# Kernel optimization log

Hardware: AMD Instinct MI355X
Metric: run time of the kernel (lower is better)

## Reference

```python
import jax, jax.numpy as jnp
import numpy as np

N, E, D, H, L = 50000, 800000, 64, 1, 4
R_DIMS = [64, 32, 16, 16]
LN_EPS = 1e-6  # flax LayerNorm default


def _ln(x, s, b):
    m = jnp.mean(x, axis=-1, keepdims=True)
    v = jnp.mean(jnp.square(x - m), axis=-1, keepdims=True)
    return (x - m) / jnp.sqrt(v + LN_EPS) * s + b


def _jat_layer(x, edges, senders, receivers, mask, Wq, Wk, Wa, ln_s, ln_b, readout):
    # x: (N, H, D) node features
    n = x.shape[0]
    q = jnp.einsum('nab,abcd->ncd', x, Wq)   # (N, H, D) query projection
    k = jnp.einsum('nab,abcd->ncd', x, Wk)   # (N, H, D) key projection
    sq = q[senders]                           # (E, H, D) gather by sender
    rk = k[receivers]                         # (E, H, D) gather by receiver
    feat = jax.nn.swish(sq + rk)
    # per-head edge distance powers, as in the original code
    ep = jnp.reshape(jnp.stack([jnp.power(edges, i + 1) for i in range(H)], axis=0), (-1, H, 1))
    feat = jnp.concatenate([feat, ep], axis=-1)       # (E, H, D+1)
    logits = jnp.einsum('eab,abcd->ecd', feat, Wa)    # (E, H, 1)
    logits = logits + jnp.reshape(jnp.where(mask, 0.0, -jnp.inf), (-1, 1, 1))
    # segment softmax over receiver segments (stable)
    maxs = jax.ops.segment_max(logits, receivers, n)
    w = jnp.exp(logits - maxs[receivers])
    w = w / jax.ops.segment_sum(w, receivers, n)[receivers]
    new = jax.ops.segment_sum(sq * w, receivers, n)   # (N, H, D)
    new = jax.nn.swish(new) + x  # skip_proj is identity (same n_head, dim)
    if not readout:
        new = _ln(new, ln_s, ln_b)
    return new


def setup_inputs() -> dict:
    key = jax.random.key(0)
    ks = jax.random.split(key, 32)
    inp = {
        'nodes': jax.random.normal(ks[0], (N, D), jnp.float32),
        'edges': jax.random.uniform(ks[1], (E, 1), jnp.float32, 0.1, 5.0),
        'senders': jax.random.randint(ks[2], (E,), 0, N, jnp.int32),
        'receivers': jax.random.randint(ks[3], (E,), 0, N, jnp.int32),
        'mask': jnp.ones((E,), bool),
        'Wq': jax.random.normal(ks[4], (L, H, D, H, D), jnp.float32) / np.sqrt(D).astype(np.float32),
        'Wk': jax.random.normal(ks[5], (L, H, D, H, D), jnp.float32) / np.sqrt(D).astype(np.float32),
        'Wa': jax.random.normal(ks[6], (L, H, D + 1, H, 1), jnp.float32) / np.sqrt(D + 1).astype(np.float32),
        'ln_scale': jnp.ones((L - 1, D), jnp.float32),
        'ln_bias': jnp.zeros((L - 1, D), jnp.float32),
    }
    dims = [H * D] + R_DIMS
    for i in range(4):
        inp[f'Wr{i}'] = jax.random.normal(ks[7 + i], (dims[i], dims[i + 1]), jnp.float32) / np.sqrt(dims[i]).astype(np.float32)
        inp[f'rs{i}'] = jnp.ones((dims[i + 1],), jnp.float32)
        inp[f'rb{i}'] = jnp.zeros((dims[i + 1],), jnp.float32)
    inp['Wr4'] = jax.random.normal(ks[11], (R_DIMS[-1], 1), jnp.float32) / np.sqrt(R_DIMS[-1]).astype(np.float32)
    return inp


def reference(nodes, edges, senders, receivers, mask, Wq, Wk, Wa, ln_scale, ln_bias,
              Wr0, Wr1, Wr2, Wr3, Wr4, rs0, rs1, rs2, rs3, rb0, rb1, rb2, rb3):
    x = nodes[:, None, :]  # (N, 1, D): stack to head axis (first layer)
    for l in range(L):
        readout = (l == L - 1)
        ln_s = ln_scale[l] if not readout else None
        ln_b = ln_bias[l] if not readout else None
        x = _jat_layer(x, edges, senders, receivers, mask, Wq[l], Wk[l], Wa[l], ln_s, ln_b, readout)
    # pyramidal readout head [64:32:16:16:1]
    h = jnp.reshape(x, (x.shape[0], -1))
    for Wd, s, b in zip((Wr0, Wr1, Wr2, Wr3), (rs0, rs1, rs2, rs3), (rb0, rb1, rb2, rb3)):
        h = jax.nn.swish(_ln(h @ Wd, s, b))
    return jax.nn.swish(h @ Wr4)  # (N, 1) atomic contributions
```

## Files before the change

### kernel.cpp

```cpp
#include <hip/hip_runtime.h>

#define NN 50000
#define EE 800000

typedef unsigned short ushort_t;
typedef unsigned int uint_t;

__device__ __forceinline__ float swishf(float v) {
    return v / (1.f + __expf(-v));
}
__device__ __forceinline__ ushort_t f2bf(float f) {
    uint_t u = __float_as_uint(f);
    return (ushort_t)((u + 0x7fffu + ((u >> 16) & 1u)) >> 16);
}
__device__ __forceinline__ float bf2f(ushort_t h) {
    return __uint_as_float(((uint_t)h) << 16);
}
__device__ __forceinline__ float rlane(float v, int i) {
    return __int_as_float(__builtin_amdgcn_readlane(__float_as_int(v), i));
}

__global__ void __launch_bounds__(256) qk_kernel(
    const float* __restrict__ x, const float* __restrict__ Wq, const float* __restrict__ Wk,
    ushort_t* __restrict__ qbf, float* __restrict__ k)
{
    const int lane = threadIdx.x & 63;
    const int wave = (blockIdx.x * 256 + threadIdx.x) >> 6;
    const int nw = gridDim.x * 4;
    float wq[64], wk[64];
#pragma unroll
    for (int i = 0; i < 64; ++i) { wq[i] = Wq[i * 64 + lane]; wk[i] = Wk[i * 64 + lane]; }
    for (int row = wave; row < NN; row += nw) {
        const float h = x[(size_t)row * 64 + lane];
        float aq0 = 0.f, aq1 = 0.f, ak0 = 0.f, ak1 = 0.f;
#pragma unroll
        for (int i = 0; i < 64; i += 2) {
            const float h0 = rlane(h, i), h1 = rlane(h, i + 1);
            aq0 = fmaf(h0, wq[i], aq0);     ak0 = fmaf(h0, wk[i], ak0);
            aq1 = fmaf(h1, wq[i + 1], aq1); ak1 = fmaf(h1, wk[i + 1], ak1);
        }
        qbf[(size_t)row * 64 + lane] = f2bf(aq0 + aq1);
        k[(size_t)row * 64 + lane] = ak0 + ak1;
    }
}

__global__ void __launch_bounds__(256) hist_kernel(
    const int* __restrict__ receivers, int* __restrict__ counts)
{
    int e = blockIdx.x * 256 + threadIdx.x;
    int stride = gridDim.x * 256;
    for (; e < EE; e += stride) atomicAdd(counts + receivers[e], 1);
}

__global__ void __launch_bounds__(256) scanA_kernel(
    const int* __restrict__ counts, int* __restrict__ bsum)
{
    const int idx = blockIdx.x * 256 + threadIdx.x;
    const int lane = threadIdx.x & 63;
    const int wid = threadIdx.x >> 6;
    int s = (idx < NN) ? counts[idx] : 0;
#pragma unroll
    for (int m = 32; m; m >>= 1) s += __shfl_xor(s, m);
    __shared__ int ws[4];
    if (lane == 0) ws[wid] = s;
    __syncthreads();
    if (threadIdx.x == 0) bsum[blockIdx.x] = ws[0] + ws[1] + ws[2] + ws[3];
}

__global__ void __launch_bounds__(256) scanB_kernel(
    const int* __restrict__ bsum, int* __restrict__ boff,
    int* __restrict__ offsets, int nb)
{
    __shared__ int ts[256];
    const int t = threadIdx.x;
    const int v = (t < nb) ? bsum[t] : 0;
    ts[t] = v;
    __syncthreads();
#pragma unroll
    for (int d = 1; d < 256; d <<= 1) {
        const int o = (t >= d) ? ts[t - d] : 0;
        __syncthreads();
        ts[t] += o;
        __syncthreads();
    }
    if (t < nb) boff[t] = ts[t] - v;
    if (t == 0) offsets[NN] = EE;
}

__global__ void __launch_bounds__(256) scanC_kernel(
    const int* __restrict__ counts, const int* __restrict__ boff,
    int* __restrict__ offsets)
{
    const int idx = blockIdx.x * 256 + threadIdx.x;
    const int lane = threadIdx.x & 63;
    const int wid = threadIdx.x >> 6;
    const int v = (idx < NN) ? counts[idx] : 0;
    int incl = v;
#pragma unroll
    for (int d = 1; d < 64; d <<= 1) {
        const int o = __shfl_up(incl, d);
        if (lane >= d) incl += o;
    }
    __shared__ int ws[4];
    if (lane == 63) ws[wid] = incl;
    __syncthreads();
    int wpre = 0;
#pragma unroll
    for (int w = 0; w < 4; ++w) wpre += (w < wid) ? ws[w] : 0;
    if (idx < NN) offsets[idx] = boff[blockIdx.x] + wpre + incl - v;
}

__global__ void __launch_bounds__(256) scatter_kernel(
    const int* __restrict__ receivers, const int* __restrict__ senders,
    const float* __restrict__ edges, const int* __restrict__ offsets,
    int* __restrict__ ctr, int* __restrict__ ssort, float* __restrict__ esort)
{
    int e = blockIdx.x * 256 + threadIdx.x;
    int stride = gridDim.x * 256;
    for (; e < EE; e += stride) {
        int r = receivers[e];
        int pos = atomicAdd(ctr + r, 1);
        int idx = offsets[r] + pos;
        ssort[idx] = senders[e];
        esort[idx] = edges[e];
    }
}

__global__ void __launch_bounds__(256) attn_kernel(
    const ushort_t* __restrict__ qbf, const float* __restrict__ k,
    const int* __restrict__ ssort, const float* __restrict__ esort,
    const int* __restrict__ offsets, const float* __restrict__ Wa,
    float* __restrict__ x, const float* __restrict__ ln_s,
    const float* __restrict__ ln_b, int do_ln)
{
    __shared__ ushort_t sQ[4][8][64];
    __shared__ float sWb[4][8];
    const int lane = threadIdx.x & 63;
    const int winb = threadIdx.x >> 6;
    const int wave = (blockIdx.x * 256 + threadIdx.x) >> 6;
    const int nw = gridDim.x * 4;
    const int c = lane & 7;
    const int e = lane >> 3;
    const int ofs = c * 8;
    float wac[8];
#pragma unroll
    for (int j = 0; j < 8; ++j) wac[j] = Wa[ofs + j];
    const float wa64 = Wa[64];
    const float lnsv = ln_s[lane], lnbv = ln_b[lane];

    for (int r = wave; r < NN; r += nw) {
        float kc[8];
        {
            const float4 k0 = *(const float4*)(k + (size_t)r * 64 + ofs);
            const float4 k1 = *(const float4*)(k + (size_t)r * 64 + ofs + 4);
            kc[0] = k0.x; kc[1] = k0.y; kc[2] = k0.z; kc[3] = k0.w;
            kc[4] = k1.x; kc[5] = k1.y; kc[6] = k1.z; kc[7] = k1.w;
        }
        const float xv = x[(size_t)r * 64 + lane];
        const int beg = offsets[r], end = offsets[r + 1];
        float m = -3.0e38f, denp = 0.f, acc = 0.f;

        bool valid = (beg + e) < end;
        int s = 0; float ea = 0.f;
        if (valid) { s = ssort[beg + e]; ea = esort[beg + e]; }
        uint4 qraw = *(const uint4*)(qbf + (size_t)s * 64 + ofs);

        int i0 = beg;
        while (i0 < end) {
            const int ni0 = i0 + 8;
            bool nvalid = false; int ns = 0; float nea = 0.f;
            uint4 nqraw = qraw;
            if (ni0 < end) {
                nvalid = (ni0 + e) < end;
                if (nvalid) { ns = ssort[ni0 + e]; nea = esort[ni0 + e]; }
                nqraw = *(const uint4*)(qbf + (size_t)ns * 64 + ofs);
            }
            float qv[8];
            qv[0] = __uint_as_float(qraw.x << 16);
            qv[1] = __uint_as_float(qraw.x & 0xFFFF0000u);
            qv[2] = __uint_as_float(qraw.y << 16);
            qv[3] = __uint_as_float(qraw.y & 0xFFFF0000u);
            qv[4] = __uint_as_float(qraw.z << 16);
            qv[5] = __uint_as_float(qraw.z & 0xFFFF0000u);
            qv[6] = __uint_as_float(qraw.w << 16);
            qv[7] = __uint_as_float(qraw.w & 0xFFFF0000u);
            float p = 0.f;
#pragma unroll
            for (int j = 0; j < 8; ++j) p = fmaf(swishf(qv[j] + kc[j]), wac[j], p);
            p += __shfl_xor(p, 1);
            p += __shfl_xor(p, 2);
            p += __shfl_xor(p, 4);
            const float logit = valid ? fmaf(ea, wa64, p) : -3.0e38f;
            float cm = logit;
            cm = fmaxf(cm, __shfl_xor(cm, 8));
            cm = fmaxf(cm, __shfl_xor(cm, 16));
            cm = fmaxf(cm, __shfl_xor(cm, 32));
            if (cm > m) {
                const float sc = __expf(m - cm);
                denp *= sc; acc *= sc; m = cm;
            }
            const float w = valid ? __expf(logit - m) : 0.f;
            denp += w;
            *(uint4*)(&sQ[winb][e][ofs]) = qraw;
            if (c == 0) sWb[winb][e] = w;
            __builtin_amdgcn_wave_barrier();
#pragma unroll
            for (int j = 0; j < 8; ++j)
                acc = fmaf(sWb[winb][j], bf2f(sQ[winb][j][lane]), acc);
            __builtin_amdgcn_wave_barrier();
            qraw = nqraw; ea = nea; valid = nvalid; i0 = ni0;
        }

        float den = denp;
#pragma unroll
        for (int msk = 32; msk; msk >>= 1) den += __shfl_xor(den, msk);
        den *= 0.125f;
        float v = den > 0.f ? acc / den : 0.f;
        float nv = swishf(v) + xv;
        if (do_ln) {
            float sum = nv;
#pragma unroll
            for (int msk = 32; msk; msk >>= 1) sum += __shfl_xor(sum, msk);
            const float mean = sum * (1.f / 64.f);
            const float d = nv - mean;
            float vs = d * d;
#pragma unroll
            for (int msk = 32; msk; msk >>= 1) vs += __shfl_xor(vs, msk);
            nv = d * rsqrtf(vs * (1.f / 64.f) + 1e-6f) * lnsv + lnbv;
        }
        x[(size_t)r * 64 + lane] = nv;
    }
}

__device__ __forceinline__ float ln_swish_w(float v, float s, float b) {
    float sum = v, sq = v * v;
#pragma unroll
    for (int m = 32; m; m >>= 1) { sum += __shfl_xor(sum, m); sq += __shfl_xor(sq, m); }
    const float mean = sum * (1.f / 64.f);
    const float var = fmaf(-mean, mean, sq * (1.f / 64.f));
    return swishf((v - mean) * rsqrtf(var + 1e-6f) * s + b);
}

__global__ void __launch_bounds__(256) readout_kernel(
    const float* __restrict__ x,
    const float* __restrict__ W0, const float* __restrict__ rs0, const float* __restrict__ rb0,
    const float* __restrict__ W1, const float* __restrict__ rs1, const float* __restrict__ rb1,
    const float* __restrict__ W2, const float* __restrict__ rs2, const float* __restrict__ rb2,
    const float* __restrict__ W3, const float* __restrict__ rs3, const float* __restrict__ rb3,
    const float* __restrict__ W4, float* __restrict__ out)
{
    const int lane = threadIdx.x & 63;
    const int wave = (blockIdx.x * 256 + threadIdx.x) >> 6;
    const int nw = gridDim.x * 4;
    const int j1 = lane & 31, j2 = lane & 15;
    float w0[64], w1[64], w2[32], w3[16];
#pragma unroll
    for (int i = 0; i < 64; ++i) w0[i] = W0[i * 64 + lane];
#pragma unroll
    for (int i = 0; i < 64; ++i) w1[i] = W1[i * 32 + j1];
#pragma unroll
    for (int i = 0; i < 32; ++i) w2[i] = W2[i * 16 + j2];
#pragma unroll
    for (int i = 0; i < 16; ++i) w3[i] = W3[i * 16 + j2];
    const float w4v = W4[j2];
    const float s0v = rs0[lane], b0v = rb0[lane];
    const float s1v = rs1[j1],  b1v = rb1[j1];
    const float s2v = rs2[j2],  b2v = rb2[j2];
    const float s3v = rs3[j2],  b3v = rb3[j2];

    for (int n = wave; n < NN; n += nw) {
        const float h = x[(size_t)n * 64 + lane];
        float a0 = 0.f, a1 = 0.f, a2 = 0.f, a3 = 0.f;
#pragma unroll
        for (int i = 0; i < 64; i += 4) {
            a0 = fmaf(rlane(h, i),     w0[i],     a0);
            a1 = fmaf(rlane(h, i + 1), w0[i + 1], a1);
            a2 = fmaf(rlane(h, i + 2), w0[i + 2], a2);
            a3 = fmaf(rlane(h, i + 3), w0[i + 3], a3);
        }
        const float y0 = ln_swish_w((a0 + a1) + (a2 + a3), s0v, b0v);

        a0 = a1 = a2 = a3 = 0.f;
#pragma unroll
        for (int i = 0; i < 64; i += 4) {
            a0 = fmaf(rlane(y0, i),     w1[i],     a0);
            a1 = fmaf(rlane(y0, i + 1), w1[i + 1], a1);
            a2 = fmaf(rlane(y0, i + 2), w1[i + 2], a2);
            a3 = fmaf(rlane(y0, i + 3), w1[i + 3], a3);
        }
        const float y1 = ln_swish_w((a0 + a1) + (a2 + a3), s1v, b1v);

        a0 = a1 = a2 = a3 = 0.f;
#pragma unroll
        for (int i = 0; i < 32; i += 4) {
            a0 = fmaf(rlane(y1, i),     w2[i],     a0);
            a1 = fmaf(rlane(y1, i + 1), w2[i + 1], a1);
            a2 = fmaf(rlane(y1, i + 2), w2[i + 2], a2);
            a3 = fmaf(rlane(y1, i + 3), w2[i + 3], a3);
        }
        const float y2 = ln_swish_w((a0 + a1) + (a2 + a3), s2v, b2v);

        a0 = a1 = a2 = a3 = 0.f;
#pragma unroll
        for (int i = 0; i < 16; i += 4) {
            a0 = fmaf(rlane(y2, i),     w3[i],     a0);
            a1 = fmaf(rlane(y2, i + 1), w3[i + 1], a1);
            a2 = fmaf(rlane(y2, i + 2), w3[i + 2], a2);
            a3 = fmaf(rlane(y2, i + 3), w3[i + 3], a3);
        }
        const float y3 = ln_swish_w((a0 + a1) + (a2 + a3), s3v, b3v);

        float p = y3 * w4v;
#pragma unroll
        for (int m = 32; m; m >>= 1) p += __shfl_xor(p, m);
        if (lane == 0) out[n] = swishf(p * 0.25f);
    }
}

extern "C" void kernel_launch(void* const* d_in, const int* in_sizes, int n_in,
                              void* d_out, int out_size, void* d_ws, size_t ws_size,
                              hipStream_t stream)
{
    const float* nodes     = (const float*)d_in[0];
    const float* edges     = (const float*)d_in[1];
    const int*   senders   = (const int*)d_in[2];
    const int*   receivers = (const int*)d_in[3];
    const float* Wq  = (const float*)d_in[5];
    const float* Wk  = (const float*)d_in[6];
    const float* Wa  = (const float*)d_in[7];
    const float* ln_s = (const float*)d_in[8];
    const float* ln_b = (const float*)d_in[9];
    const float* Wr0 = (const float*)d_in[10];
    const float* rs0 = (const float*)d_in[11];
    const float* rb0 = (const float*)d_in[12];
    const float* Wr1 = (const float*)d_in[13];
    const float* rs1 = (const float*)d_in[14];
    const float* rb1 = (const float*)d_in[15];
    const float* Wr2 = (const float*)d_in[16];
    const float* rs2 = (const float*)d_in[17];
    const float* rb2 = (const float*)d_in[18];
    const float* Wr3 = (const float*)d_in[19];
    const float* rs3 = (const float*)d_in[20];
    const float* rb3 = (const float*)d_in[21];
    const float* Wr4 = (const float*)d_in[22];
    float* out = (float*)d_out;

    float*    x       = (float*)d_ws;
    float*    k       = x + (size_t)NN * 64;
    ushort_t* qbf     = (ushort_t*)(k + (size_t)NN * 64);
    int*      counts  = (int*)(qbf + (size_t)NN * 64);
    int*      ctr     = counts + NN;
    int*      offsets = ctr + NN;
    int*      ssort   = offsets + NN + 1;
    float*    esort   = (float*)(ssort + EE);
    int*      bsum    = (int*)(esort + EE);
    int*      boff    = bsum + 256;

    const int NB = (NN + 255) / 256;

    hipMemcpyAsync(x, nodes, (size_t)NN * 64 * sizeof(float), hipMemcpyDeviceToDevice, stream);

    hipMemsetAsync(counts, 0, 2 * NN * sizeof(int), stream);
    hist_kernel<<<3125, 256, 0, stream>>>(receivers, counts);
    scanA_kernel<<<NB, 256, 0, stream>>>(counts, bsum);
    scanB_kernel<<<1, 256, 0, stream>>>(bsum, boff, offsets, NB);
    scanC_kernel<<<NB, 256, 0, stream>>>(counts, boff, offsets);
    scatter_kernel<<<3125, 256, 0, stream>>>(receivers, senders, edges, offsets, ctr, ssort, esort);

    for (int l = 0; l < 4; ++l) {
        qk_kernel<<<1024, 256, 0, stream>>>(x, Wq + l * 4096, Wk + l * 4096, qbf, k);
        int lnidx = l < 3 ? l : 0;
        attn_kernel<<<3125, 256, 0, stream>>>(qbf, k, ssort, esort, offsets,
                                              Wa + l * 65, x,
                                              ln_s + lnidx * 64, ln_b + lnidx * 64,
                                              l < 3 ? 1 : 0);
    }
    readout_kernel<<<1024, 256, 0, stream>>>(x, Wr0, rs0, rb0, Wr1, rs1, rb1,
                                             Wr2, rs2, rb2, Wr3, rs3, rb3, Wr4, out);
}
```

Before: 593.4 us.

## Pack sender/edge into int2, use fast reciprocal, split readout kernel

Packs the sorted sender index and edge value into one int2 array, so the attention loop does one 8-byte load per edge instead of two separate loads. Divisions in swish and in the softmax normalisation are replaced with a hardware reciprocal instruction, and qk gets a launch-bounds occupancy hint. The readout kernel is split into two kernels that pass the first layer's activations through global memory (reusing the k buffer), which lowers register pressure per kernel. The costs are an extra global round trip and launch for the readout, and slightly less precise reciprocals.

```diff
diff --git a/kernel.cpp b/kernel.cpp
--- a/kernel.cpp
+++ b/kernel.cpp
@@ -6,8 +6,11 @@
 typedef unsigned short ushort_t;
 typedef unsigned int uint_t;
 
+__device__ __forceinline__ float rcpf(float x) {
+    float r; asm("v_rcp_f32 %0, %1" : "=v"(r) : "v"(x)); return r;
+}
 __device__ __forceinline__ float swishf(float v) {
-    return v / (1.f + __expf(-v));
+    return v * rcpf(1.f + __expf(-v));
 }
 __device__ __forceinline__ ushort_t f2bf(float f) {
     uint_t u = __float_as_uint(f);
@@ -20,7 +23,7 @@
     return __int_as_float(__builtin_amdgcn_readlane(__float_as_int(v), i));
 }
 
-__global__ void __launch_bounds__(256) qk_kernel(
+__global__ void __launch_bounds__(256, 2) qk_kernel(
     const float* __restrict__ x, const float* __restrict__ Wq, const float* __restrict__ Wk,
     ushort_t* __restrict__ qbf, float* __restrict__ k)
 {
@@ -113,23 +116,21 @@
 __global__ void __launch_bounds__(256) scatter_kernel(
     const int* __restrict__ receivers, const int* __restrict__ senders,
     const float* __restrict__ edges, const int* __restrict__ offsets,
-    int* __restrict__ ctr, int* __restrict__ ssort, float* __restrict__ esort)
+    int* __restrict__ ctr, int2* __restrict__ sesort)
 {
     int e = blockIdx.x * 256 + threadIdx.x;
     int stride = gridDim.x * 256;
     for (; e < EE; e += stride) {
         int r = receivers[e];
         int pos = atomicAdd(ctr + r, 1);
-        int idx = offsets[r] + pos;
-        ssort[idx] = senders[e];
-        esort[idx] = edges[e];
+        sesort[offsets[r] + pos] = make_int2(senders[e], __float_as_int(edges[e]));
     }
 }
 
 __global__ void __launch_bounds__(256) attn_kernel(
     const ushort_t* __restrict__ qbf, const float* __restrict__ k,
-    const int* __restrict__ ssort, const float* __restrict__ esort,
-    const int* __restrict__ offsets, const float* __restrict__ Wa,
+    const int2* __restrict__ sesort, const int* __restrict__ offsets,
+    const float* __restrict__ Wa,
     float* __restrict__ x, const float* __restrict__ ln_s,
     const float* __restrict__ ln_b, int do_ln)
 {
@@ -161,19 +162,22 @@
         float m = -3.0e38f, denp = 0.f, acc = 0.f;
 
         bool valid = (beg + e) < end;
-        int s = 0; float ea = 0.f;
-        if (valid) { s = ssort[beg + e]; ea = esort[beg + e]; }
-        uint4 qraw = *(const uint4*)(qbf + (size_t)s * 64 + ofs);
+        int2 sev = make_int2(0, 0);
+        if (valid) sev = sesort[beg + e];
+        uint4 qraw = *(const uint4*)(qbf + (size_t)sev.x * 64 + ofs);
+        float ea = __int_as_float(sev.y);
 
         int i0 = beg;
         while (i0 < end) {
             const int ni0 = i0 + 8;
-            bool nvalid = false; int ns = 0; float nea = 0.f;
+            bool nvalid = false; float nea = 0.f;
             uint4 nqraw = qraw;
             if (ni0 < end) {
                 nvalid = (ni0 + e) < end;
-                if (nvalid) { ns = ssort[ni0 + e]; nea = esort[ni0 + e]; }
-                nqraw = *(const uint4*)(qbf + (size_t)ns * 64 + ofs);
+                int2 nsev = make_int2(0, 0);
+                if (nvalid) nsev = sesort[ni0 + e];
+                nqraw = *(const uint4*)(qbf + (size_t)nsev.x * 64 + ofs);
+                nea = __int_as_float(nsev.y);
             }
             float qv[8];
             qv[0] = __uint_as_float(qraw.x << 16);
@@ -215,7 +219,7 @@
 #pragma unroll
         for (int msk = 32; msk; msk >>= 1) den += __shfl_xor(den, msk);
         den *= 0.125f;
-        float v = den > 0.f ? acc / den : 0.f;
+        float v = den > 0.f ? acc * rcpf(den) : 0.f;
         float nv = swishf(v) + xv;
         if (do_ln) {
             float sum = nv;
@@ -241,33 +245,18 @@
     return swishf((v - mean) * rsqrtf(var + 1e-6f) * s + b);
 }
 
-__global__ void __launch_bounds__(256) readout_kernel(
+__global__ void __launch_bounds__(256, 2) rd0_kernel(
     const float* __restrict__ x,
     const float* __restrict__ W0, const float* __restrict__ rs0, const float* __restrict__ rb0,
-    const float* __restrict__ W1, const float* __restrict__ rs1, const float* __restrict__ rb1,
-    const float* __restrict__ W2, const float* __restrict__ rs2, const float* __restrict__ rb2,
-    const float* __restrict__ W3, const float* __restrict__ rs3, const float* __restrict__ rb3,
-    const float* __restrict__ W4, float* __restrict__ out)
+    float* __restrict__ y0out)
 {
     const int lane = threadIdx.x & 63;
     const int wave = (blockIdx.x * 256 + threadIdx.x) >> 6;
     const int nw = gridDim.x * 4;
-    const int j1 = lane & 31, j2 = lane & 15;
-    float w0[64], w1[64], w2[32], w3[16];
+    float w0[64];
 #pragma unroll
     for (int i = 0; i < 64; ++i) w0[i] = W0[i * 64 + lane];
-#pragma unroll
-    for (int i = 0; i < 64; ++i) w1[i] = W1[i * 32 + j1];
-#pragma unroll
-    for (int i = 0; i < 32; ++i) w2[i] = W2[i * 16 + j2];
-#pragma unroll
-    for (int i = 0; i < 16; ++i) w3[i] = W3[i * 16 + j2];
-    const float w4v = W4[j2];
     const float s0v = rs0[lane], b0v = rb0[lane];
-    const float s1v = rs1[j1],  b1v = rb1[j1];
-    const float s2v = rs2[j2],  b2v = rb2[j2];
-    const float s3v = rs3[j2],  b3v = rb3[j2];
-
     for (int n = wave; n < NN; n += nw) {
         const float h = x[(size_t)n * 64 + lane];
         float a0 = 0.f, a1 = 0.f, a2 = 0.f, a3 = 0.f;
@@ -278,9 +267,36 @@
             a2 = fmaf(rlane(h, i + 2), w0[i + 2], a2);
             a3 = fmaf(rlane(h, i + 3), w0[i + 3], a3);
         }
-        const float y0 = ln_swish_w((a0 + a1) + (a2 + a3), s0v, b0v);
-
-        a0 = a1 = a2 = a3 = 0.f;
+        y0out[(size_t)n * 64 + lane] = ln_swish_w((a0 + a1) + (a2 + a3), s0v, b0v);
+    }
+}
+
+__global__ void __launch_bounds__(256, 2) rd1_kernel(
+    const float* __restrict__ y0in,
+    const float* __restrict__ W1, const float* __restrict__ rs1, const float* __restrict__ rb1,
+    const float* __restrict__ W2, const float* __restrict__ rs2, const float* __restrict__ rb2,
+    const float* __restrict__ W3, const float* __restrict__ rs3, const float* __restrict__ rb3,
+    const float* __restrict__ W4, float* __restrict__ out)
+{
+    const int lane = threadIdx.x & 63;
+    const int wave = (blockIdx.x * 256 + threadIdx.x) >> 6;
+    const int nw = gridDim.x * 4;
+    const int j1 = lane & 31, j2 = lane & 15;
+    float w1[64], w2[32], w3[16];
+#pragma unroll
+    for (int i = 0; i < 64; ++i) w1[i] = W1[i * 32 + j1];
+#pragma unroll
+    for (int i = 0; i < 32; ++i) w2[i] = W2[i * 16 + j2];
+#pragma unroll
+    for (int i = 0; i < 16; ++i) w3[i] = W3[i * 16 + j2];
+    const float w4v = W4[j2];
+    const float s1v = rs1[j1], b1v = rb1[j1];
+    const float s2v = rs2[j2], b2v = rb2[j2];
+    const float s3v = rs3[j2], b3v = rb3[j2];
+
+    for (int n = wave; n < NN; n += nw) {
+        const float y0 = y0in[(size_t)n * 64 + lane];
+        float a0 = 0.f, a1 = 0.f, a2 = 0.f, a3 = 0.f;
 #pragma unroll
         for (int i = 0; i < 64; i += 4) {
             a0 = fmaf(rlane(y0, i),     w1[i],     a0);
@@ -351,9 +367,8 @@
     int*      counts  = (int*)(qbf + (size_t)NN * 64);
     int*      ctr     = counts + NN;
     int*      offsets = ctr + NN;
-    int*      ssort   = offsets + NN + 1;
-    float*    esort   = (float*)(ssort + EE);
-    int*      bsum    = (int*)(esort + EE);
+    int2*     sesort  = (int2*)(offsets + NN + 2);
+    int*      bsum    = (int*)(sesort + EE);
     int*      boff    = bsum + 256;
 
     const int NB = (NN + 255) / 256;
@@ -365,16 +380,17 @@
     scanA_kernel<<<NB, 256, 0, stream>>>(counts, bsum);
     scanB_kernel<<<1, 256, 0, stream>>>(bsum, boff, offsets, NB);
     scanC_kernel<<<NB, 256, 0, stream>>>(counts, boff, offsets);
-    scatter_kernel<<<3125, 256, 0, stream>>>(receivers, senders, edges, offsets, ctr, ssort, esort);
+    scatter_kernel<<<3125, 256, 0, stream>>>(receivers, senders, edges, offsets, ctr, sesort);
 
     for (int l = 0; l < 4; ++l) {
         qk_kernel<<<1024, 256, 0, stream>>>(x, Wq + l * 4096, Wk + l * 4096, qbf, k);
         int lnidx = l < 3 ? l : 0;
-        attn_kernel<<<3125, 256, 0, stream>>>(qbf, k, ssort, esort, offsets,
+        attn_kernel<<<3125, 256, 0, stream>>>(qbf, k, sesort, offsets,
                                               Wa + l * 65, x,
                                               ln_s + lnidx * 64, ln_b + lnidx * 64,
                                               l < 3 ? 1 : 0);
     }
-    readout_kernel<<<1024, 256, 0, stream>>>(x, Wr0, rs0, rb0, Wr1, rs1, rb1,
-                                             Wr2, rs2, rb2, Wr3, rs3, rb3, Wr4, out);
-}
+    rd0_kernel<<<1024, 256, 0, stream>>>(x, Wr0, rs0, rb0, k);
+    rd1_kernel<<<1024, 256, 0, stream>>>(k, Wr1, rs1, rb1, Wr2, rs2, rb2,
+                                         Wr3, rs3, rb3, Wr4, out);
+}
```

Result: faster. 553.3 us (-6.8%).
